# Optimization experiments

Hardware: AMD Instinct MI355X
Metric: run time of the kernel (lower is better)

The kernel has to match this reference:

```python
import jax, jax.numpy as jnp
import numpy as np

N_ROWS = 4096   # output dim (c_3)
N_COLS = 4096   # input dim (c_4)
NNZ = 4194304


def setup_inputs() -> dict:
    key = jax.random.key(0)
    k1, k2, k3, k4 = jax.random.split(key, 4)
    x = jax.random.normal(k1, (4, 2048, N_COLS), dtype=jnp.float32)
    values = jax.random.normal(k2, (NNZ,), dtype=jnp.float32)
    col_idx = jax.random.randint(k3, (NNZ,), 0, N_COLS, dtype=jnp.int32)
    row_ids = jnp.sort(jax.random.randint(k4, (NNZ,), 0, N_ROWS, dtype=jnp.int32))
    return {"x": x, "values": values, "col_idx": col_idx, "row_ids": row_ids}


def reference(x, values, col_idx, row_ids):
    # Faithful math of macko_spmv.multiply applied to every flattened row of x:
    #   out[..., r] = sum_k values[k] * x[..., col_idx[k]]  where row_ids[k] == r
    # Instead of N separate sparse matvecs (the original Python loop), scatter the
    # compressed weights into the dense matrix once and do a single batched GEMM.
    W = jnp.zeros((N_ROWS, N_COLS), dtype=values.dtype).at[row_ids, col_idx].add(values)
    return jnp.einsum('bsh,oh->bso', x, W)  # [B, S, N_ROWS]
```

## Files before the change

### kernel.cpp

```cpp
#include <hip/hip_runtime.h>


#define M_DIM 8192
#define K_DIM 4096
#define N_DIM 4096
#define NNZ   4194304
#define FXSCALE 1048576.0f
#define FXINV  (1.0f / 1048576.0f)

typedef __bf16 bf16x8 __attribute__((ext_vector_type(8)));
typedef float  floatx4 __attribute__((ext_vector_type(4)));
typedef unsigned short ushort8 __attribute__((ext_vector_type(8)));

__device__ __forceinline__ unsigned short f32_to_bf16(float f) {
  unsigned int u = __float_as_uint(f);
  u += 0x7FFFu + ((u >> 16) & 1u);
  return (unsigned short)(u >> 16);
}

__device__ __forceinline__ void async_copy16(const void* g, void* l) {
  __builtin_amdgcn_global_load_lds(
      (const __attribute__((address_space(1))) void*)g,
      (__attribute__((address_space(3))) void*)l,
      16, 0, 0);
}

__global__ void row_start_kernel(const int* __restrict__ rows,
                                 int* __restrict__ row_start) {
  int i = blockIdx.x * blockDim.x + threadIdx.x;
  if (i > NNZ) return;
  int cur  = (i < NNZ) ? rows[i] : N_DIM;
  int prev = (i > 0) ? rows[i - 1] : -1;
  for (int r = prev + 1; r <= cur; ++r) row_start[r] = i;
}

__global__ __launch_bounds__(256) void build_w_kernel(
    const float* __restrict__ vals,
    const int* __restrict__ cols,
    const int* __restrict__ row_start,
    unsigned short* __restrict__ Wb) {
  __shared__ int wrow[K_DIM];

  const int r = blockIdx.x;
  for (int i = threadIdx.x; i < K_DIM; i += 256) wrow[i] = 0;
  __syncthreads();

  const int start = row_start[r];
  const int end   = row_start[r + 1];
  for (int i = start + threadIdx.x; i < end; i += 256)
    atomicAdd(&wrow[cols[i]], (int)lrintf(vals[i] * FXSCALE));
  __syncthreads();

  ushort8* dst = (ushort8*)(Wb + (size_t)r * K_DIM);
  for (int i = threadIdx.x; i < K_DIM / 8; i += 256) {
    const int* s = &wrow[i * 8];
    ushort8 o;
#pragma unroll
    for (int j = 0; j < 8; j++) o[j] = f32_to_bf16((float)s[j] * FXINV);
    dst[i] = o;
  }
}

__global__ void cvt_kernel(const float4* __restrict__ in,
                           ushort4* __restrict__ out, int n4) {
  int i = blockIdx.x * blockDim.x + threadIdx.x;
  if (i < n4) {
    float4 v = in[i];
    ushort4 o;
    o.x = f32_to_bf16(v.x);
    o.y = f32_to_bf16(v.y);
    o.z = f32_to_bf16(v.z);
    o.w = f32_to_bf16(v.w);
    out[i] = o;
  }
}

__global__ __launch_bounds__(256, 2) void gemm_bt(
    const unsigned short* __restrict__ A,
    const unsigned short* __restrict__ B,
    float* __restrict__ C) {
  __shared__ unsigned short As[128 * 32];
  __shared__ unsigned short Bs[128 * 32];

  const int tid  = threadIdx.x;
  const int wave = tid >> 6;
  const int lane = tid & 63;
  const int quad = lane >> 4;
  const int l16  = lane & 15;

  const int m0 = blockIdx.y * 128;
  const int n0 = blockIdx.x * 128;

  const int wm = (wave >> 1) * 64;
  const int wn = (wave & 1) * 64;

  floatx4 acc[4][4];
#pragma unroll
  for (int i = 0; i < 4; i++)
#pragma unroll
    for (int j = 0; j < 4; j++) acc[i][j] = (floatx4){0.f, 0.f, 0.f, 0.f};

  const int srow = lane >> 2;
  const int scol = (lane & 3) * 8;

  const unsigned short* Ag0 = A + (size_t)(m0 +      wave * 16 + srow) * K_DIM + scol;
  const unsigned short* Ag1 = A + (size_t)(m0 + 64 + wave * 16 + srow) * K_DIM + scol;
  const unsigned short* Bg0 = B + (size_t)(n0 +      wave * 16 + srow) * K_DIM + scol;
  const unsigned short* Bg1 = B + (size_t)(n0 + 64 + wave * 16 + srow) * K_DIM + scol;

  unsigned short* Al0 = &As[(wave * 16) * 32] + lane * 8;
  unsigned short* Al1 = &As[(64 + wave * 16) * 32] + lane * 8;
  unsigned short* Bl0 = &Bs[(wave * 16) * 32] + lane * 8;
  unsigned short* Bl1 = &Bs[(64 + wave * 16) * 32] + lane * 8;

  for (int kt = 0; kt < K_DIM; kt += 32) {
    __syncthreads();
    async_copy16(Ag0 + kt, Al0);
    async_copy16(Ag1 + kt, Al1);
    async_copy16(Bg0 + kt, Bl0);
    async_copy16(Bg1 + kt, Bl1);
    __syncthreads();

    bf16x8 af[4], bf[4];
#pragma unroll
    for (int t = 0; t < 4; t++) {
      af[t] = *(const bf16x8*)&As[(wm + t * 16 + l16) * 32 + quad * 8];
      bf[t] = *(const bf16x8*)&Bs[(wn + t * 16 + l16) * 32 + quad * 8];
    }
#pragma unroll
    for (int tm = 0; tm < 4; tm++)
#pragma unroll
      for (int tn = 0; tn < 4; tn++)
        acc[tm][tn] = __builtin_amdgcn_mfma_f32_16x16x32_bf16(
            af[tm], bf[tn], acc[tm][tn], 0, 0, 0);
  }

#pragma unroll
  for (int tm = 0; tm < 4; tm++) {
#pragma unroll
    for (int r = 0; r < 4; r++) {
      const int row = m0 + wm + tm * 16 + quad * 4 + r;
      float* Cp = C + (size_t)row * N_DIM + n0 + wn + l16;
#pragma unroll
      for (int tn = 0; tn < 4; tn++) Cp[tn * 16] = acc[tm][tn][r];
    }
  }
}

extern "C" void kernel_launch(void* const* d_in, const int* in_sizes, int n_in,
                              void* d_out, int out_size, void* d_ws, size_t ws_size,
                              hipStream_t stream) {
  const float* x       = (const float*)d_in[0];
  const float* values  = (const float*)d_in[1];
  const int*   col_idx = (const int*)d_in[2];
  const int*   row_ids = (const int*)d_in[3];
  float* out = (float*)d_out;

  unsigned short* Wb = (unsigned short*)d_ws;
  unsigned short* Xb = (unsigned short*)((char*)d_ws + ((size_t)32 << 20));
  int* row_start     = (int*)((char*)d_ws + ((size_t)96 << 20));

  const int x4 = M_DIM * K_DIM / 4;

  row_start_kernel<<<(NNZ + 256) / 256, 256, 0, stream>>>(row_ids, row_start);
  cvt_kernel<<<(x4 + 255) / 256, 256, 0, stream>>>((const float4*)x, (ushort4*)Xb, x4);
  build_w_kernel<<<N_DIM, 256, 0, stream>>>(values, col_idx, row_start, Wb);

  dim3 grid(N_DIM / 128, M_DIM / 128);
  gemm_bt<<<grid, 256, 0, stream>>>(Xb, Wb, out);
}
```

Baseline: 548.0 us.

## Enlarge GEMM tile to 256x256 with 4-stage async LDS pipeline and swizzle

The GEMM moves from 128x128 tiles with 4 waves and a single LDS buffer to 256x256 tiles with 8 waves. It uses a 4-deep ring of LDS buffers filled by async global_load_lds, paced by explicit vmcnt waits and barriers so loads for later k-tiles overlap MFMA work. It also adds an XOR swizzle on LDS rows to avoid bank conflicts, and raises wave priority around the MFMA block. The aim is to cut the per-iteration double-barrier stalls and raise arithmetic intensity, at the cost of more registers (8x4 accumulators) and 64KB of LDS, which may limit occupancy.

```diff
diff --git a/kernel.cpp b/kernel.cpp
--- a/kernel.cpp
+++ b/kernel.cpp
@@ -7,6 +7,10 @@
 #define NNZ   4194304
 #define FXSCALE 1048576.0f
 #define FXINV  (1.0f / 1048576.0f)
+
+#define BK 32
+#define NT (K_DIM / BK)
+#define TILE_US (256 * BK)
 
 typedef __bf16 bf16x8 __attribute__((ext_vector_type(8)));
 typedef float  floatx4 __attribute__((ext_vector_type(4)));
@@ -75,68 +79,108 @@
   }
 }
 
-__global__ __launch_bounds__(256, 2) void gemm_bt(
+__global__ __launch_bounds__(512, 2) void gemm_bt(
     const unsigned short* __restrict__ A,
     const unsigned short* __restrict__ B,
     float* __restrict__ C) {
-  __shared__ unsigned short As[128 * 32];
-  __shared__ unsigned short Bs[128 * 32];
+  __shared__ unsigned short As[4 * TILE_US];
+  __shared__ unsigned short Bs[4 * TILE_US];
 
   const int tid  = threadIdx.x;
-  const int wave = tid >> 6;
+  const int wid  = tid >> 6;
   const int lane = tid & 63;
   const int quad = lane >> 4;
   const int l16  = lane & 15;
 
-  const int m0 = blockIdx.y * 128;
-  const int n0 = blockIdx.x * 128;
-
-  const int wm = (wave >> 1) * 64;
-  const int wn = (wave & 1) * 64;
-
-  floatx4 acc[4][4];
-#pragma unroll
-  for (int i = 0; i < 4; i++)
+  const int m0 = blockIdx.y * 256;
+  const int n0 = blockIdx.x * 256;
+  const int wm = (wid >> 2) * 128;
+  const int wn = (wid & 3) * 64;
+
+  const int p  = tid;
+  const int sr = ((p >> 3) << 1) | (((p >> 2) ^ (p >> 4)) & 1);
+  const int sq = (p & 3) ^ (sr & 3);
+
+  const unsigned short* Ag0 = A + (size_t)(m0 + sr) * K_DIM + sq * 8;
+  const unsigned short* Ag1 = Ag0 + (size_t)128 * K_DIM;
+  const unsigned short* Bg0 = B + (size_t)(n0 + sr) * K_DIM + sq * 8;
+  const unsigned short* Bg1 = Bg0 + (size_t)128 * K_DIM;
+
+  unsigned short* Al0 = &As[(wid * 16) * BK] + lane * 8;
+  unsigned short* Al1 = Al0 + 128 * BK;
+  unsigned short* Bl0 = &Bs[(wid * 16) * BK] + lane * 8;
+  unsigned short* Bl1 = Bl0 + 128 * BK;
+
+  int offA[8], offB[4];
+#pragma unroll
+  for (int t = 0; t < 8; ++t) {
+    const int row = wm + t * 16 + l16;
+    offA[t] = ((row * 4 + quad) ^ (row & 7)) << 3;
+  }
+#pragma unroll
+  for (int t = 0; t < 4; ++t) {
+    const int row = wn + t * 16 + l16;
+    offB[t] = ((row * 4 + quad) ^ (row & 7)) << 3;
+  }
+
+  floatx4 acc[8][4];
+#pragma unroll
+  for (int i = 0; i < 8; i++)
 #pragma unroll
     for (int j = 0; j < 4; j++) acc[i][j] = (floatx4){0.f, 0.f, 0.f, 0.f};
 
-  const int srow = lane >> 2;
-  const int scol = (lane & 3) * 8;
-
-  const unsigned short* Ag0 = A + (size_t)(m0 +      wave * 16 + srow) * K_DIM + scol;
-  const unsigned short* Ag1 = A + (size_t)(m0 + 64 + wave * 16 + srow) * K_DIM + scol;
-  const unsigned short* Bg0 = B + (size_t)(n0 +      wave * 16 + srow) * K_DIM + scol;
-  const unsigned short* Bg1 = B + (size_t)(n0 + 64 + wave * 16 + srow) * K_DIM + scol;
-
-  unsigned short* Al0 = &As[(wave * 16) * 32] + lane * 8;
-  unsigned short* Al1 = &As[(64 + wave * 16) * 32] + lane * 8;
-  unsigned short* Bl0 = &Bs[(wave * 16) * 32] + lane * 8;
-  unsigned short* Bl1 = &Bs[(64 + wave * 16) * 32] + lane * 8;
-
-  for (int kt = 0; kt < K_DIM; kt += 32) {
-    __syncthreads();
-    async_copy16(Ag0 + kt, Al0);
-    async_copy16(Ag1 + kt, Al1);
-    async_copy16(Bg0 + kt, Bl0);
-    async_copy16(Bg1 + kt, Bl1);
-    __syncthreads();
-
-    bf16x8 af[4], bf[4];
-#pragma unroll
-    for (int t = 0; t < 4; t++) {
-      af[t] = *(const bf16x8*)&As[(wm + t * 16 + l16) * 32 + quad * 8];
-      bf[t] = *(const bf16x8*)&Bs[(wn + t * 16 + l16) * 32 + quad * 8];
-    }
-#pragma unroll
-    for (int tm = 0; tm < 4; tm++)
-#pragma unroll
-      for (int tn = 0; tn < 4; tn++)
-        acc[tm][tn] = __builtin_amdgcn_mfma_f32_16x16x32_bf16(
-            af[tm], bf[tn], acc[tm][tn], 0, 0, 0);
-  }
-
-#pragma unroll
-  for (int tm = 0; tm < 4; tm++) {
+#define STAGE(t_) do {                                   \
+    const int b_  = (t_) & 3;                            \
+    const int kt_ = (t_) * BK;                           \
+    async_copy16(Ag0 + kt_, Al0 + b_ * TILE_US);         \
+    async_copy16(Ag1 + kt_, Al1 + b_ * TILE_US);         \
+    async_copy16(Bg0 + kt_, Bl0 + b_ * TILE_US);         \
+    async_copy16(Bg1 + kt_, Bl1 + b_ * TILE_US);         \
+  } while (0)
+
+#define COMPUTE(t_) do {                                                      \
+    const unsigned short* Ab_ = &As[((t_) & 3) * TILE_US];                    \
+    const unsigned short* Bb_ = &Bs[((t_) & 3) * TILE_US];                    \
+    bf16x8 af_[8], bf_[4];                                                    \
+    _Pragma("unroll")                                                         \
+    for (int i_ = 0; i_ < 8; ++i_) af_[i_] = *(const bf16x8*)(Ab_ + offA[i_]);\
+    _Pragma("unroll")                                                         \
+    for (int j_ = 0; j_ < 4; ++j_) bf_[j_] = *(const bf16x8*)(Bb_ + offB[j_]);\
+    __builtin_amdgcn_s_setprio(1);                                            \
+    _Pragma("unroll")                                                         \
+    for (int i_ = 0; i_ < 8; ++i_)                                            \
+      _Pragma("unroll")                                                       \
+      for (int j_ = 0; j_ < 4; ++j_)                                          \
+        acc[i_][j_] = __builtin_amdgcn_mfma_f32_16x16x32_bf16(                \
+            af_[i_], bf_[j_], acc[i_][j_], 0, 0, 0);                          \
+    __builtin_amdgcn_s_setprio(0);                                            \
+  } while (0)
+
+  STAGE(0);
+  STAGE(1);
+  STAGE(2);
+
+  for (int t = 0; t < NT - 3; ++t) {
+    asm volatile("s_waitcnt vmcnt(8)" ::: "memory");
+    asm volatile("s_barrier" ::: "memory");
+    STAGE(t + 3);
+    COMPUTE(t);
+  }
+  asm volatile("s_waitcnt vmcnt(8)" ::: "memory");
+  asm volatile("s_barrier" ::: "memory");
+  COMPUTE(NT - 3);
+  asm volatile("s_waitcnt vmcnt(4)" ::: "memory");
+  asm volatile("s_barrier" ::: "memory");
+  COMPUTE(NT - 2);
+  asm volatile("s_waitcnt vmcnt(0)" ::: "memory");
+  asm volatile("s_barrier" ::: "memory");
+  COMPUTE(NT - 1);
+
+#undef STAGE
+#undef COMPUTE
+
+#pragma unroll
+  for (int tm = 0; tm < 8; tm++) {
 #pragma unroll
     for (int r = 0; r < 4; r++) {
       const int row = m0 + wm + tm * 16 + quad * 4 + r;
@@ -166,6 +210,6 @@
   cvt_kernel<<<(x4 + 255) / 256, 256, 0, stream>>>((const float4*)x, (ushort4*)Xb, x4);
   build_w_kernel<<<N_DIM, 256, 0, stream>>>(values, col_idx, row_start, Wb);
 
-  dim3 grid(N_DIM / 128, M_DIM / 128);
-  gemm_bt<<<grid, 256, 0, stream>>>(Xb, Wb, out);
-}
+  dim3 grid(N_DIM / 256, M_DIM / 256);
+  gemm_bt<<<grid, 512, 0, stream>>>(Xb, Wb, out);
+}
```

After: 581.4 us. 1.06x slower.

## Rewrite GEMM as 256x256 tile, double-buffered, swizzled-LDS pipelined kernel

Applied to the files above, without the earlier changes.

Replaces the simple 128x128 GEMM, which issued a single-buffered async copy and synced twice per 32-wide K step, with a 512-thread 256x256 tile kernel. It uses BK=64, double-buffered LDS with XOR-swizzled layout, and interleaves half-tile async loads with MFMA phases under explicit barriers and waitcnts. The kernel also remaps block indices for better L2 locality and raises MFMA priority with setprio. This aims to hide global load latency and raise MFMA utilization. The cost is high register pressure from 32 accumulators per lane, plus brittle hand-tuned waitcnt counts.

```diff
diff --git a/kernel.cpp b/kernel.cpp
--- a/kernel.cpp
+++ b/kernel.cpp
@@ -7,6 +7,10 @@
 #define NNZ   4194304
 #define FXSCALE 1048576.0f
 #define FXINV  (1.0f / 1048576.0f)
+
+#define BKT 64
+#define NTIL (K_DIM / BKT)
+#define ABUF 16384
 
 typedef __bf16 bf16x8 __attribute__((ext_vector_type(8)));
 typedef float  floatx4 __attribute__((ext_vector_type(4)));
@@ -75,74 +79,201 @@
   }
 }
 
-__global__ __launch_bounds__(256, 2) void gemm_bt(
+#define BAR()   asm volatile("s_barrier" ::: "memory")
+#define LGKM0() do { asm volatile("s_waitcnt lgkmcnt(0)" ::: "memory"); \
+                     __builtin_amdgcn_sched_barrier(0); } while (0)
+#define VMW6()  asm volatile("s_waitcnt vmcnt(6)" ::: "memory")
+#define VMW0()  asm volatile("s_waitcnt vmcnt(0)" ::: "memory")
+
+#define STAGEH(Gb_, Lb_, h_, kt_) do {                                          \
+  async_copy16((Gb_) + (size_t)((h_)*128 +      srow) * K_DIM + (kt_),          \
+               (Lb_) + (h_)*8192 +        tid * 8);                             \
+  async_copy16((Gb_) + (size_t)((h_)*128 + 64 + srow) * K_DIM + (kt_),          \
+               (Lb_) + (h_)*8192 + 4096 + tid * 8);                             \
+} while (0)
+
+#define RD_A(Ab_, mb_) do {                                                     \
+  _Pragma("unroll")                                                             \
+  for (int m_ = 0; m_ < 4; ++m_) {                                              \
+    af[m_][0] = *(const bf16x8*)((Ab_) + offA[(mb_) + m_][0]);                  \
+    af[m_][1] = *(const bf16x8*)((Ab_) + offA[(mb_) + m_][1]);                  \
+  }                                                                             \
+} while (0)
+
+#define RD_B(Bb_, nb_) do {                                                     \
+  _Pragma("unroll")                                                             \
+  for (int n_ = 0; n_ < 2; ++n_) {                                              \
+    bf[(nb_) + n_][0] = *(const bf16x8*)((Bb_) + offB[(nb_) + n_][0]);          \
+    bf[(nb_) + n_][1] = *(const bf16x8*)((Bb_) + offB[(nb_) + n_][1]);          \
+  }                                                                             \
+} while (0)
+
+#define MM(mb_, nb_) do {                                                       \
+  __builtin_amdgcn_s_setprio(1);                                                \
+  _Pragma("unroll")                                                             \
+  for (int m_ = 0; m_ < 4; ++m_)                                                \
+    _Pragma("unroll")                                                           \
+    for (int n_ = 0; n_ < 2; ++n_) {                                            \
+      acc[(mb_) + m_][(nb_) + n_] = __builtin_amdgcn_mfma_f32_16x16x32_bf16(    \
+          af[m_][0], bf[(nb_) + n_][0], acc[(mb_) + m_][(nb_) + n_], 0, 0, 0);  \
+      acc[(mb_) + m_][(nb_) + n_] = __builtin_amdgcn_mfma_f32_16x16x32_bf16(    \
+          af[m_][1], bf[(nb_) + n_][1], acc[(mb_) + m_][(nb_) + n_], 0, 0, 0);  \
+    }                                                                           \
+  __builtin_amdgcn_s_setprio(0);                                                \
+} while (0)
+
+__global__ __launch_bounds__(512, 2) void gemm_bt(
     const unsigned short* __restrict__ A,
     const unsigned short* __restrict__ B,
     float* __restrict__ C) {
-  __shared__ unsigned short As[128 * 32];
-  __shared__ unsigned short Bs[128 * 32];
+  __shared__ __attribute__((aligned(16))) unsigned short LDS[4][ABUF];
 
   const int tid  = threadIdx.x;
-  const int wave = tid >> 6;
+  const int wid  = tid >> 6;
   const int lane = tid & 63;
   const int quad = lane >> 4;
   const int l16  = lane & 15;
-
-  const int m0 = blockIdx.y * 128;
-  const int n0 = blockIdx.x * 128;
-
-  const int wm = (wave >> 1) * 64;
-  const int wn = (wave & 1) * 64;
-
-  floatx4 acc[4][4];
-#pragma unroll
-  for (int i = 0; i < 4; i++)
+  const int mh   = wid >> 2;
+  const int w32  = wid & 3;
+
+  int wg = blockIdx.x;
+  wg = (wg & 7) * 64 + (wg >> 3);
+  const int n0 = (wg & 15) * 256;
+  const int m0 = (wg >> 4) * 256;
+
+  const int srow = tid >> 3;
+  const int sblk = ((tid & 7) ^ ((tid >> 3) & 7)) * 8;
+  const unsigned short* Abase = A + (size_t)m0 * K_DIM + sblk;
+  const unsigned short* Bbase = B + (size_t)n0 * K_DIM + sblk;
+
+  int offA[8][2], offB[4][2];
+#pragma unroll
+  for (int m = 0; m < 8; ++m) {
+    const int r = (m < 4 ? mh * 64 + m * 16 : 128 + mh * 64 + (m - 4) * 16) + l16;
+#pragma unroll
+    for (int h = 0; h < 2; ++h)
+      offA[m][h] = r * 64 + (((h * 4 + quad) ^ (r & 7)) * 8);
+  }
+#pragma unroll
+  for (int n = 0; n < 4; ++n) {
+    const int r = (n < 2 ? w32 * 32 + n * 16 : 128 + w32 * 32 + (n - 2) * 16) + l16;
+#pragma unroll
+    for (int h = 0; h < 2; ++h)
+      offB[n][h] = r * 64 + (((h * 4 + quad) ^ (r & 7)) * 8);
+  }
+
+  floatx4 acc[8][4];
+#pragma unroll
+  for (int i = 0; i < 8; i++)
 #pragma unroll
     for (int j = 0; j < 4; j++) acc[i][j] = (floatx4){0.f, 0.f, 0.f, 0.f};
 
-  const int srow = lane >> 2;
-  const int scol = (lane & 3) * 8;
-
-  const unsigned short* Ag0 = A + (size_t)(m0 +      wave * 16 + srow) * K_DIM + scol;
-  const unsigned short* Ag1 = A + (size_t)(m0 + 64 + wave * 16 + srow) * K_DIM + scol;
-  const unsigned short* Bg0 = B + (size_t)(n0 +      wave * 16 + srow) * K_DIM + scol;
-  const unsigned short* Bg1 = B + (size_t)(n0 + 64 + wave * 16 + srow) * K_DIM + scol;
-
-  unsigned short* Al0 = &As[(wave * 16) * 32] + lane * 8;
-  unsigned short* Al1 = &As[(64 + wave * 16) * 32] + lane * 8;
-  unsigned short* Bl0 = &Bs[(wave * 16) * 32] + lane * 8;
-  unsigned short* Bl1 = &Bs[(64 + wave * 16) * 32] + lane * 8;
-
-  for (int kt = 0; kt < K_DIM; kt += 32) {
-    __syncthreads();
-    async_copy16(Ag0 + kt, Al0);
-    async_copy16(Ag1 + kt, Al1);
-    async_copy16(Bg0 + kt, Bl0);
-    async_copy16(Bg1 + kt, Bl1);
-    __syncthreads();
-
-    bf16x8 af[4], bf[4];
-#pragma unroll
-    for (int t = 0; t < 4; t++) {
-      af[t] = *(const bf16x8*)&As[(wm + t * 16 + l16) * 32 + quad * 8];
-      bf[t] = *(const bf16x8*)&Bs[(wn + t * 16 + l16) * 32 + quad * 8];
-    }
-#pragma unroll
-    for (int tm = 0; tm < 4; tm++)
-#pragma unroll
-      for (int tn = 0; tn < 4; tn++)
-        acc[tm][tn] = __builtin_amdgcn_mfma_f32_16x16x32_bf16(
-            af[tm], bf[tn], acc[tm][tn], 0, 0, 0);
-  }
-
-#pragma unroll
-  for (int tm = 0; tm < 4; tm++) {
+  bf16x8 af[4][2], bf[4][2];
+
+  unsigned short* A0L = &LDS[0][0];
+  unsigned short* B0L = &LDS[1][0];
+  unsigned short* A1L = &LDS[2][0];
+  unsigned short* B1L = &LDS[3][0];
+
+  STAGEH(Abase, A0L, 0, 0);
+  STAGEH(Bbase, B0L, 0, 0);
+  STAGEH(Abase, A0L, 1, 0);
+  STAGEH(Bbase, B0L, 1, 0);
+  STAGEH(Abase, A1L, 0, BKT);
+  STAGEH(Bbase, B1L, 0, BKT);
+  STAGEH(Abase, A1L, 1, BKT);
+  VMW6();
+  BAR();
+
+  for (int i = 0; i < NTIL / 2 - 1; ++i) {
+    const int ktE = (2 * i) * BKT;
+    RD_A(A0L, 0); RD_B(B0L, 0);
+    STAGEH(Bbase, B1L, 1, ktE + BKT);
+    BAR(); LGKM0();
+    MM(0, 0);
+    BAR();
+    RD_B(B0L, 2);
+    STAGEH(Abase, A0L, 0, ktE + 2 * BKT);
+    BAR(); LGKM0();
+    MM(0, 2);
+    BAR();
+    RD_A(A0L, 4);
+    STAGEH(Bbase, B0L, 0, ktE + 2 * BKT);
+    BAR(); LGKM0();
+    MM(4, 0);
+    BAR();
+    STAGEH(Abase, A0L, 1, ktE + 2 * BKT);
+    BAR();
+    MM(4, 2);
+    VMW6();
+    BAR();
+    RD_A(A1L, 0); RD_B(B1L, 0);
+    STAGEH(Bbase, B0L, 1, ktE + 2 * BKT);
+    BAR(); LGKM0();
+    MM(0, 0);
+    BAR();
+    RD_B(B1L, 2);
+    STAGEH(Abase, A1L, 0, ktE + 3 * BKT);
+    BAR(); LGKM0();
+    MM(0, 2);
+    BAR();
+    RD_A(A1L, 4);
+    STAGEH(Bbase, B1L, 0, ktE + 3 * BKT);
+    BAR(); LGKM0();
+    MM(4, 0);
+    BAR();
+    STAGEH(Abase, A1L, 1, ktE + 3 * BKT);
+    BAR();
+    MM(4, 2);
+    VMW6();
+    BAR();
+  }
+
+  {
+    const int ktE = (NTIL - 2) * BKT;
+    RD_A(A0L, 0); RD_B(B0L, 0);
+    STAGEH(Bbase, B1L, 1, ktE + BKT);
+    BAR(); LGKM0();
+    MM(0, 0);
+    BAR();
+    RD_B(B0L, 2);
+    BAR(); LGKM0();
+    MM(0, 2);
+    BAR();
+    RD_A(A0L, 4);
+    BAR(); LGKM0();
+    MM(4, 0);
+    BAR();
+    MM(4, 2);
+    VMW0();
+    BAR();
+    RD_A(A1L, 0); RD_B(B1L, 0);
+    BAR(); LGKM0();
+    MM(0, 0);
+    BAR();
+    RD_B(B1L, 2);
+    BAR(); LGKM0();
+    MM(0, 2);
+    BAR();
+    RD_A(A1L, 4);
+    BAR(); LGKM0();
+    MM(4, 0);
+    BAR();
+    MM(4, 2);
+  }
+
+#pragma unroll
+  for (int m = 0; m < 8; m++) {
+    const int mrow = (m < 4 ? mh * 64 + m * 16 : 128 + mh * 64 + (m - 4) * 16);
 #pragma unroll
     for (int r = 0; r < 4; r++) {
-      const int row = m0 + wm + tm * 16 + quad * 4 + r;
-      float* Cp = C + (size_t)row * N_DIM + n0 + wn + l16;
-#pragma unroll
-      for (int tn = 0; tn < 4; tn++) Cp[tn * 16] = acc[tm][tn][r];
+      const int row = m0 + mrow + quad * 4 + r;
+      float* Cp = C + (size_t)row * N_DIM + n0 + l16;
+#pragma unroll
+      for (int n = 0; n < 4; n++) {
+        const int ncol = (n < 2 ? w32 * 32 + n * 16 : 128 + w32 * 32 + (n - 2) * 16);
+        Cp[ncol] = acc[m][n][r];
+      }
     }
   }
 }
@@ -166,6 +297,5 @@
   cvt_kernel<<<(x4 + 255) / 256, 256, 0, stream>>>((const float4*)x, (ushort4*)Xb, x4);
   build_w_kernel<<<N_DIM, 256, 0, stream>>>(values, col_idx, row_start, Wb);
 
-  dim3 grid(N_DIM / 128, M_DIM / 128);
-  gemm_bt<<<grid, 256, 0, stream>>>(Xb, Wb, out);
-}
+  gemm_bt<<<dim3(512), 512, 0, stream>>>(Xb, Wb, out);
+}
```

New measurement: 466.9 us. 14.8% less time.
